# Kernel optimization log

Measured on AMD Instinct MI355X. Metric: run time of the kernel, lower is better.

Reference implementation:

```python
import jax, jax.numpy as jnp
import numpy as np
import math
from jax import lax

D_MODEL = 128
N_HEADS = 8
D_HEAD = D_MODEL // N_HEADS
D_FF = 4 * D_MODEL
KERNEL = 25  # moving_avg kernel size
N_LAYERS = 2
EPS = 1e-5


def moving_avg(x):
    # x: [B, L, D]; replicate-pad (KERNEL-1)//2 at both ends, window mean (AvgPool1d stride 1)
    p = (KERNEL - 1) // 2
    xp = jnp.concatenate([jnp.repeat(x[:, :1], p, axis=1), x, jnp.repeat(x[:, -1:], p, axis=1)], axis=1)
    s = lax.reduce_window(xp, 0.0, lax.add, (1, KERNEL, 1), (1, 1, 1), 'VALID')
    return s / KERNEL


def series_decomp(x):
    mm = moving_avg(x)
    return x - mm, mm


def autocorrelation(q, k, v):
    # q,k,v: [B, L, H, E]; FFT-based period correlation + top-k time-delay aggregation (training path)
    B, L, H, E = q.shape
    top_k = int(1 * math.log(L))  # factor=1
    qf = jnp.fft.rfft(q.transpose(0, 2, 3, 1), axis=-1)
    kf = jnp.fft.rfft(k.transpose(0, 2, 3, 1), axis=-1)
    corr = jnp.fft.irfft(qf * jnp.conj(kf), n=L, axis=-1)  # [B, H, E, L]
    vals = v.transpose(0, 2, 3, 1)                          # [B, H, E, L]
    mean_value = corr.mean(axis=(1, 2))                     # [B, L]
    _, index = lax.top_k(mean_value.mean(axis=0), top_k)    # [top_k], lags shared over batch
    weights = mean_value[:, index]                          # [B, top_k]
    tmp_corr = jax.nn.softmax(weights, axis=-1)
    agg = jnp.zeros_like(vals)
    for i in range(top_k):  # static small loop (top_k = 8)
        pattern = jnp.roll(vals, -index[i], axis=-1)
        agg = agg + pattern * tmp_corr[:, i][:, None, None, None]
    return agg.transpose(0, 3, 1, 2)  # [B, L, H, E]


def attn_layer(x, w, b):
    # w: [4, D, D] (q,k,v,out torch-Linear weights), b: [4, D]
    B, L, D = x.shape
    q = (jnp.einsum('bld,ed->ble', x, w[0]) + b[0]).reshape(B, L, N_HEADS, D_HEAD)
    k = (jnp.einsum('bld,ed->ble', x, w[1]) + b[1]).reshape(B, L, N_HEADS, D_HEAD)
    v = (jnp.einsum('bld,ed->ble', x, w[2]) + b[2]).reshape(B, L, N_HEADS, D_HEAD)
    o = autocorrelation(q, k, v).reshape(B, L, D)
    return jnp.einsum('bld,ed->ble', o, w[3]) + b[3]


def encoder_layer(x, w, b, w1, w2):
    x = x + attn_layer(x, w, b)
    x, _ = series_decomp(x)
    y = jax.nn.gelu(jnp.einsum('bld,fd->blf', x, w1), approximate=False)  # conv1 (k=1, no bias)
    y = jnp.einsum('blf,df->bld', y, w2)                                   # conv2 (k=1, no bias)
    res, _ = series_decomp(x + y)
    return res


def reference(x_enc, emb_w, attn_w, attn_b, ffn_w1, ffn_w2, norm_g, norm_b, fc1_w, fc1_b, fc2_w, fc2_b):
    # token embedding: Conv1d(C -> D, kernel 3, circular padding, no bias)
    xc = x_enc.transpose(0, 2, 1)  # [B, C, L]
    xc = jnp.concatenate([xc[:, :, -1:], xc, xc[:, :, :1]], axis=-1)
    h = lax.conv_general_dilated(xc, emb_w, (1,), 'VALID', dimension_numbers=('NCH', 'OIH', 'NCH'))
    h = h.transpose(0, 2, 1)  # [B, L, D]
    for l in range(N_LAYERS):
        h = encoder_layer(h, attn_w[l], attn_b[l], ffn_w1[l], ffn_w2[l])
    # my_Layernorm: LayerNorm then subtract time-mean
    mu = h.mean(axis=-1, keepdims=True)
    var = ((h - mu) ** 2).mean(axis=-1, keepdims=True)
    ln = (h - mu) / jnp.sqrt(var + EPS) * norm_g + norm_b
    h = ln - ln.mean(axis=1, keepdims=True)
    # head: gelu -> mean pool over time -> MLP
    h = jax.nn.gelu(h, approximate=False).mean(axis=1)  # [B, D]
    h = jax.nn.relu(jnp.einsum('bd,hd->bh', h, fc1_w) + fc1_b)
    return jnp.einsum('bh,ch->bc', h, fc2_w) + fc2_b


def setup_inputs() -> dict:
    key = jax.random.key(0)
    ks = jax.random.split(key, 8)
    B, L, C, NC, FC = 32, 4096, 12, 5, 128
    s = 0.02
    return {
        'x_enc': jax.random.normal(ks[0], (B, L, C), jnp.float32),
        'emb_w': jax.random.normal(ks[1], (D_MODEL, C, 3), jnp.float32) * s,
        'attn_w': jax.random.normal(ks[2], (N_LAYERS, 4, D_MODEL, D_MODEL), jnp.float32) * s,
        'attn_b': jnp.zeros((N_LAYERS, 4, D_MODEL), jnp.float32),
        'ffn_w1': jax.random.normal(ks[3], (N_LAYERS, D_FF, D_MODEL), jnp.float32) * s,
        'ffn_w2': jax.random.normal(ks[4], (N_LAYERS, D_MODEL, D_FF), jnp.float32) * s,
        'norm_g': jnp.ones((D_MODEL,), jnp.float32),
        'norm_b': jnp.zeros((D_MODEL,), jnp.float32),
        'fc1_w': jax.random.normal(ks[5], (FC, D_MODEL), jnp.float32) * s,
        'fc1_b': jnp.zeros((FC,), jnp.float32),
        'fc2_w': jax.random.normal(ks[6], (NC, FC), jnp.float32) * s,
        'fc2_b': jnp.zeros((NC,), jnp.float32),
    }
```

## Files before the change

### kernel.cpp

```cpp
#include <hip/hip_runtime.h>
#include <math.h>

#define L_SEQ 4096
#define BATCH 32
#define DM 128

typedef short short8 __attribute__((ext_vector_type(8)));
typedef short short4v __attribute__((ext_vector_type(4)));
typedef float f32x4 __attribute__((ext_vector_type(4)));

__device__ __forceinline__ float gelu_f(float x) {
    return 0.5f * x * (1.0f + erff(x * 0.70710678118654752f));
}
__device__ __forceinline__ float gelu_fast(float x) {
    float ax = fabsf(x);
    if (ax < 1.0f) {
        float z = x * 0.70710678118654752f;
        float z2 = z * z;
        float p = 1.0f + z2 * (-0.333333333f + z2 * (0.1f + z2 * (-0.0238095238f +
                  z2 * (4.62962963e-3f + z2 * (-7.57575758e-4f)))));
        return 0.5f * x * (1.0f + 1.1283791670955126f * z * p);
    }
    return 0.5f * x * (1.0f + erff(x * 0.70710678118654752f));
}
__device__ __forceinline__ unsigned short f2b(float f) {
    unsigned u = __float_as_uint(f);
    u += 0x7fffu + ((u >> 16) & 1u);
    return (unsigned short)(u >> 16);
}
__device__ __forceinline__ float b2f(unsigned short h) {
    return __uint_as_float(((unsigned)h) << 16);
}

__global__ __launch_bounds__(256) void kembed(const float* __restrict__ x,
                                              const float* __restrict__ w,
                                              float* __restrict__ h) {
    __shared__ float xs[130][12];
    __shared__ float wsm[128][37];
    int b = blockIdx.x >> 5;
    int lt = blockIdx.x & 31;
    int l0 = lt * 128;
    int tid = threadIdx.x;
    for (int i = tid; i < 130 * 12; i += 256) {
        int r = i / 12, c = i - r * 12;
        int gl = (l0 - 1 + r + 4096) & 4095;
        xs[r][c] = x[((size_t)b * 4096 + gl) * 12 + c];
    }
    for (int i = tid; i < 128 * 36; i += 256) {
        int o = i / 36, j = i - o * 36;
        wsm[o][j] = w[i];
    }
    __syncthreads();
    int o = tid & 127, lh = tid >> 7;
    float wr[36];
#pragma unroll
    for (int j = 0; j < 36; j++) wr[j] = wsm[o][j];
    int base_r = lh * 64;
    float ring[4][12];
#pragma unroll
    for (int c = 0; c < 12; c++) { ring[0][c] = xs[base_r][c]; ring[1][c] = xs[base_r + 1][c]; }
    float* hp = h + ((size_t)b * 4096 + l0 + lh * 64) * 128 + o;
#pragma unroll 4
    for (int st = 0; st < 64; st++) {
        int s0 = st & 3, s1 = (st + 1) & 3, s2 = (st + 2) & 3;
#pragma unroll
        for (int c = 0; c < 12; c++) ring[s2][c] = xs[base_r + st + 2][c];
        float s = 0.f;
#pragma unroll
        for (int c = 0; c < 12; c++)
            s += wr[c * 3 + 0] * ring[s0][c] + wr[c * 3 + 1] * ring[s1][c] + wr[c * 3 + 2] * ring[s2][c];
        hp[(size_t)st * 128] = s;
    }
}

__global__ __launch_bounds__(256) void kprepw(const float* __restrict__ w1,
                                              const float* __restrict__ w2,
                                              const float* __restrict__ attn_w,
                                              unsigned short* __restrict__ w1img,
                                              unsigned short* __restrict__ w2img,
                                              unsigned short* __restrict__ qkh,
                                              unsigned short* __restrict__ qkl,
                                              unsigned short* __restrict__ voimg) {
    int t = blockIdx.x * 256 + threadIdx.x;
    if (t < 262144) {
        int layer = t >> 17; int rem = t & 131071;
        if (rem < 65536) {
            int R = rem >> 7, x = rem & 127;
            int g = x >> 3, j = x & 7;
            int srcc = ((g ^ (R & 7)) << 3) + j;
            w1img[(size_t)layer * 65536 + rem] = f2b(w1[(size_t)layer * 65536 + R * 128 + srcc]);
        } else {
            int r2 = rem - 65536;
            int c = r2 >> 13; int D = (r2 >> 6) & 127; int x = r2 & 63;
            int g = x >> 3, j = x & 7;
            int srcf = c * 64 + ((g ^ (D & 7)) << 3) + j;
            w2img[(size_t)layer * 65536 + r2] = f2b(w2[(size_t)layer * 65536 + D * 512 + srcf]);
        }
    } else if (t < 327680) {
        int t2 = t - 262144;
        int layer = t2 >> 15; int rem = t2 & 32767;
        int y = rem >> 14; int rem2 = rem & 16383;
        int r64 = rem2 >> 7; int x = rem2 & 127;
        int r = r64 & 63;
        int g = x >> 3, j = x & 7;
        int srcc = ((g ^ (r & 7)) << 3) + j;
        float v = attn_w[(size_t)layer * 65536 + y * 16384 + r64 * 128 + srcc];
        unsigned short hh = f2b(v);
        qkh[t2] = hh;
        qkl[t2] = f2b(v - b2f(hh));
    } else {
        int t3 = t - 327680;
        int layer = t3 >> 15; int rem = t3 & 32767;
        int mat = rem >> 14; int rem2 = rem & 16383;
        int r = rem2 >> 7; int x = rem2 & 127;
        int g = x >> 3, j = x & 7;
        int srcc = ((g ^ (r & 7)) << 3) + j;
        voimg[t3] = f2b(attn_w[(size_t)layer * 65536 + (2 + mat) * 16384 + r * 128 + srcc]);
    }
}

__global__ __launch_bounds__(256, 2) void kgemm_qkb(const float* __restrict__ A,
                                                    const unsigned short* __restrict__ qkh,
                                                    const unsigned short* __restrict__ qkl,
                                                    const float* __restrict__ ab,
                                                    unsigned short* __restrict__ CTb) {
    __shared__ __align__(16) char smem[65536];
    short* Ah = (short*)smem;
    short* Al = (short*)(smem + 16384);
    short* Wh = (short*)(smem + 32768);
    short* Wl = (short*)(smem + 49152);
    int role = blockIdx.x;
    int y = role >> 1, half = role & 1;
    const unsigned short* wh = qkh + y * 16384 + half * 8192;
    const unsigned short* wl = qkl + y * 16384 + half * 8192;
    const float* bias = ab + y * 128 + half * 64;
    int row0 = blockIdx.y * 64;
    int tid = threadIdx.x;
#pragma unroll
    for (int u = 0; u < 4; u++) {
        int task = tid + u * 256;
        int r = task >> 4, cg = task & 15;
        int dst = r * 128 + ((cg ^ (r & 7)) << 3);
        const float* src = A + ((size_t)(row0 + r)) * 128 + cg * 8;
        float4 xa = *(const float4*)src, ya = *(const float4*)(src + 4);
        float av[8] = {xa.x, xa.y, xa.z, xa.w, ya.x, ya.y, ya.z, ya.w};
        short8 hi, lo;
#pragma unroll
        for (int j = 0; j < 8; j++) {
            unsigned short h = f2b(av[j]);
            hi[j] = (short)h; lo[j] = (short)f2b(av[j] - b2f(h));
        }
        *(short8*)(Ah + dst) = hi; *(short8*)(Al + dst) = lo;
        int lin = r * 128 + cg * 8;
        *(short8*)(Wh + lin) = *(const short8*)(wh + lin);
        *(short8*)(Wl + lin) = *(const short8*)(wl + lin);
    }
    __syncthreads();
    int l = tid & 63; int w = tid >> 6; int wm = w >> 1, wn = w & 1;
    f32x4 acc[2][2];
#pragma unroll
    for (int i = 0; i < 2; i++)
#pragma unroll
        for (int j = 0; j < 2; j++) acc[i][j] = (f32x4){0.f, 0.f, 0.f, 0.f};
#pragma unroll
    for (int ks = 0; ks < 4; ks++) {
        int cg = ks * 4 + (l >> 4);
        short8 ah[2], al2[2], bh[2], bl[2];
#pragma unroll
        for (int mi = 0; mi < 2; mi++) {
            int rm = wm * 32 + mi * 16 + (l & 15);
            int off = rm * 128 + ((cg ^ (rm & 7)) << 3);
            ah[mi] = *(short8*)(Ah + off); al2[mi] = *(short8*)(Al + off);
        }
#pragma unroll
        for (int ni = 0; ni < 2; ni++) {
            int rn = wn * 32 + ni * 16 + (l & 15);
            int off = rn * 128 + ((cg ^ (rn & 7)) << 3);
            bh[ni] = *(short8*)(Wh + off); bl[ni] = *(short8*)(Wl + off);
        }
#pragma unroll
        for (int mi = 0; mi < 2; mi++)
#pragma unroll
            for (int ni = 0; ni < 2; ni++) {
                acc[mi][ni] = __builtin_amdgcn_mfma_f32_16x16x32_bf16(ah[mi], bh[ni], acc[mi][ni], 0, 0, 0);
                acc[mi][ni] = __builtin_amdgcn_mfma_f32_16x16x32_bf16(ah[mi], bl[ni], acc[mi][ni], 0, 0, 0);
                acc[mi][ni] = __builtin_amdgcn_mfma_f32_16x16x32_bf16(al2[mi], bh[ni], acc[mi][ni], 0, 0, 0);
            }
    }
    __syncthreads();
    float* Dsh = (float*)smem;
#pragma unroll
    for (int mi = 0; mi < 2; mi++)
#pragma unroll
        for (int ni = 0; ni < 2; ni++)
#pragma unroll
            for (int rr = 0; rr < 4; rr++) {
                int m = wm * 32 + mi * 16 + (l >> 4) * 4 + rr;
                int n = wn * 32 + ni * 16 + (l & 15);
                Dsh[n * 68 + m] = acc[mi][ni][rr] + bias[n];
            }
    __syncthreads();
    int b = row0 >> 12; int l0 = row0 & 4095;
    int cb = y * 128 + half * 64;
#pragma unroll
    for (int u = 0; u < 4; u++) {
        int task = tid + u * 256;
        int c = task >> 4, m4 = (task & 15) * 4;
        float4 v = *(float4*)&Dsh[c * 68 + m4];
        short4v o;
        o[0] = (short)f2b(v.x); o[1] = (short)f2b(v.y);
        o[2] = (short)f2b(v.z); o[3] = (short)f2b(v.w);
        *(short4v*)&CTb[((size_t)(b * 256 + cb + c)) * 4096 + l0 + m4] = o;
    }
}

template <int AT, int EPI>
__global__ __launch_bounds__(256, 2) void kgemm_mfma(const void* __restrict__ Ap,
                                                     const unsigned short* __restrict__ Wimg,
                                                     const float* __restrict__ bias,
                                                     const float* __restrict__ res,
                                                     const float* __restrict__ tcb,
                                                     const int* __restrict__ idxb,
                                                     void* __restrict__ outp) {
    __shared__ __align__(16) char smem[65536];
    short* As = (short*)smem;
    short* Ws = (short*)(smem + 32768);
    int tid = threadIdx.x;
    size_t row0 = (size_t)blockIdx.x * 128;
#pragma unroll
    for (int u = 0; u < 8; u++) {
        int g = tid + u * 256;
        int r = g >> 4, cg = g & 15;
        int dsti = r * 128 + ((cg ^ (r & 7)) << 3);
        short8 v;
        if (AT == 0) {
            const float* src = (const float*)Ap + (row0 + r) * 128 + cg * 8;
            float4 x = *(const float4*)src, y = *(const float4*)(src + 4);
            v[0] = f2b(x.x); v[1] = f2b(x.y); v[2] = f2b(x.z); v[3] = f2b(x.w);
            v[4] = f2b(y.x); v[5] = f2b(y.y); v[6] = f2b(y.z); v[7] = f2b(y.w);
        } else {
            const unsigned short* Vb = (const unsigned short*)Ap;
            int b = (int)(row0 >> 12);
            int l0 = (int)(row0 & 4095);
            float accv[8];
#pragma unroll
            for (int j = 0; j < 8; j++) accv[j] = 0.f;
#pragma unroll
            for (int i = 0; i < 8; i++) {
                float wgt = tcb[b * 8 + i];
                int lr = (l0 + r + idxb[i]) & 4095;
                short8 vv = *(const short8*)(Vb + ((size_t)(b * 4096 + lr)) * 128 + cg * 8);
#pragma unroll
                for (int j = 0; j < 8; j++) accv[j] += wgt * b2f((unsigned short)vv[j]);
            }
#pragma unroll
            for (int j = 0; j < 8; j++) v[j] = (short)f2b(accv[j]);
        }
        *(short8*)(As + dsti) = v;
        int lin = r * 128 + cg * 8;
        *(short8*)(Ws + lin) = *(const short8*)(Wimg + lin);
    }
    __syncthreads();
    int l = tid & 63; int w = tid >> 6; int wm = w >> 1, wn = w & 1;
    f32x4 acc[4][4];
#pragma unroll
    for (int i = 0; i < 4; i++)
#pragma unroll
        for (int j = 0; j < 4; j++) acc[i][j] = (f32x4){0.f, 0.f, 0.f, 0.f};
#pragma unroll
    for (int ks = 0; ks < 4; ks++) {
        int cg = ks * 4 + (l >> 4);
        short8 af[4], bf[4];
#pragma unroll
        for (int mi = 0; mi < 4; mi++) {
            int rm = wm * 64 + mi * 16 + (l & 15);
            af[mi] = *(short8*)(As + rm * 128 + ((cg ^ (rm & 7)) << 3));
        }
#pragma unroll
        for (int ni = 0; ni < 4; ni++) {
            int rn = wn * 64 + ni * 16 + (l & 15);
            bf[ni] = *(short8*)(Ws + rn * 128 + ((cg ^ (rn & 7)) << 3));
        }
#pragma unroll
        for (int mi = 0; mi < 4; mi++)
#pragma unroll
            for (int ni = 0; ni < 4; ni++)
                acc[mi][ni] = __builtin_amdgcn_mfma_f32_16x16x32_bf16(af[mi], bf[ni], acc[mi][ni], 0, 0, 0);
    }
    __syncthreads();
    float* Dsh = (float*)smem;
#pragma unroll
    for (int mi = 0; mi < 4; mi++)
#pragma unroll
        for (int ni = 0; ni < 4; ni++)
#pragma unroll
            for (int rr = 0; rr < 4; rr++)
                Dsh[(wm * 64 + mi * 16 + (l >> 4) * 4 + rr) * 128 + wn * 64 + ni * 16 + (l & 15)] = acc[mi][ni][rr];
    __syncthreads();
#pragma unroll
    for (int u = 0; u < 8; u++) {
        int g = tid + u * 256;
        int r = g >> 4, c8 = (g & 15) * 8;
        float vv[8];
#pragma unroll
        for (int j = 0; j < 8; j++) vv[j] = Dsh[r * 128 + c8 + j] + bias[c8 + j];
        if (EPI == 1) {
            const float* rp = res + (row0 + r) * 128 + c8;
#pragma unroll
            for (int j = 0; j < 8; j++) vv[j] += rp[j];
            float* op = (float*)outp + (row0 + r) * 128 + c8;
            *(float4*)op = make_float4(vv[0], vv[1], vv[2], vv[3]);
            *(float4*)(op + 4) = make_float4(vv[4], vv[5], vv[6], vv[7]);
        } else {
            short8 ov;
#pragma unroll
            for (int j = 0; j < 8; j++) ov[j] = (short)f2b(vv[j]);
            *(short8*)((short*)outp + (row0 + r) * 128 + c8) = ov;
        }
    }
}

#define LOADW(FB) do { \
    _Pragma("unroll") \
    for (int u = 0; u < 4; u++) { \
        int task = tid + u * 256; \
        int r = task >> 4, cg = task & 15; \
        p1[u] = *(const short8*)(w1img + ((size_t)((FB) * 64 + r)) * 128 + cg * 8); \
        int r2 = task >> 3, cg2 = task & 7; \
        p2[u] = *(const short8*)(w2img + ((size_t)((FB) * 128 + r2)) * 64 + cg2 * 8); \
    } \
} while (0)

__global__ __launch_bounds__(256, 2) void kffn_mfma(const float* __restrict__ xs,
                                                    const unsigned short* __restrict__ w1img,
                                                    const unsigned short* __restrict__ w2img,
                                                    float* __restrict__ outp) {
    __shared__ __align__(16) char smem[81920];
    short* xsl = (short*)smem;
    short* w1t = (short*)(smem + 32768);
    short* tt  = (short*)(smem + 49152);
    short* w2t = (short*)(smem + 65536);
    int tid = threadIdx.x;
    size_t row0 = (size_t)blockIdx.x * 128;
#pragma unroll
    for (int u = 0; u < 8; u++) {
        int g = tid + u * 256;
        int r = g >> 4, cg = g & 15;
        const float* src = xs + (row0 + r) * 128 + cg * 8;
        float4 x = *(const float4*)src, y = *(const float4*)(src + 4);
        short8 v;
        v[0] = f2b(x.x); v[1] = f2b(x.y); v[2] = f2b(x.z); v[3] = f2b(x.w);
        v[4] = f2b(y.x); v[5] = f2b(y.y); v[6] = f2b(y.z); v[7] = f2b(y.w);
        *(short8*)(xsl + r * 128 + ((cg ^ (r & 7)) << 3)) = v;
    }
    int l = tid & 63; int w = tid >> 6; int wm = w >> 1, wn = w & 1;
    f32x4 acc2[4][4];
#pragma unroll
    for (int i = 0; i < 4; i++)
#pragma unroll
        for (int j = 0; j < 4; j++) acc2[i][j] = (f32x4){0.f, 0.f, 0.f, 0.f};
    short8 p1[4], p2[4];
    LOADW(0);
    for (int fb = 0; fb < 8; fb++) {
        __syncthreads();
#pragma unroll
        for (int u = 0; u < 4; u++) {
            int task = tid + u * 256;
            int r = task >> 4, cg = task & 15;
            *(short8*)(w1t + r * 128 + cg * 8) = p1[u];
            int r2 = task >> 3, cg2 = task & 7;
            *(short8*)(w2t + r2 * 64 + cg2 * 8) = p2[u];
        }
        __syncthreads();
        if (fb < 7) LOADW(fb + 1);
        f32x4 a1[4][2];
#pragma unroll
        for (int i = 0; i < 4; i++)
#pragma unroll
            for (int j = 0; j < 2; j++) a1[i][j] = (f32x4){0.f, 0.f, 0.f, 0.f};
#pragma unroll
        for (int ks = 0; ks < 4; ks++) {
            int cg = ks * 4 + (l >> 4);
            short8 af[4], bf[2];
#pragma unroll
            for (int mi = 0; mi < 4; mi++) {
                int rm = wm * 64 + mi * 16 + (l & 15);
                af[mi] = *(short8*)(xsl + rm * 128 + ((cg ^ (rm & 7)) << 3));
            }
#pragma unroll
            for (int ni = 0; ni < 2; ni++) {
                int rn = wn * 32 + ni * 16 + (l & 15);
                bf[ni] = *(short8*)(w1t + rn * 128 + ((cg ^ (rn & 7)) << 3));
            }
#pragma unroll
            for (int mi = 0; mi < 4; mi++)
#pragma unroll
                for (int ni = 0; ni < 2; ni++)
                    a1[mi][ni] = __builtin_amdgcn_mfma_f32_16x16x32_bf16(af[mi], bf[ni], a1[mi][ni], 0, 0, 0);
        }
#pragma unroll
        for (int mi = 0; mi < 4; mi++)
#pragma unroll
            for (int ni = 0; ni < 2; ni++)
#pragma unroll
                for (int rr = 0; rr < 4; rr++) {
                    int m = wm * 64 + mi * 16 + (l >> 4) * 4 + rr;
                    int f = wn * 32 + ni * 16 + (l & 15);
                    tt[m * 64 + (((f >> 3) ^ (m & 7)) << 3) + (f & 7)] = (short)f2b(gelu_fast(a1[mi][ni][rr]));
                }
        __syncthreads();
#pragma unroll
        for (int ks = 0; ks < 2; ks++) {
            int cg = ks * 4 + (l >> 4);
            short8 af[4], bf[4];
#pragma unroll
            for (int mi = 0; mi < 4; mi++) {
                int rm = wm * 64 + mi * 16 + (l & 15);
                af[mi] = *(short8*)(tt + rm * 64 + ((cg ^ (rm & 7)) << 3));
            }
#pragma unroll
            for (int ni = 0; ni < 4; ni++) {
                int rn = wn * 64 + ni * 16 + (l & 15);
                bf[ni] = *(short8*)(w2t + rn * 64 + ((cg ^ (rn & 7)) << 3));
            }
#pragma unroll
            for (int mi = 0; mi < 4; mi++)
#pragma unroll
                for (int ni = 0; ni < 4; ni++)
                    acc2[mi][ni] = __builtin_amdgcn_mfma_f32_16x16x32_bf16(af[mi], bf[ni], acc2[mi][ni], 0, 0, 0);
        }
    }
    __syncthreads();
    float* Dsh = (float*)smem;
#pragma unroll
    for (int mi = 0; mi < 4; mi++)
#pragma unroll
        for (int ni = 0; ni < 4; ni++)
#pragma unroll
            for (int rr = 0; rr < 4; rr++)
                Dsh[(wm * 64 + mi * 16 + (l >> 4) * 4 + rr) * 128 + wn * 64 + ni * 16 + (l & 15)] = acc2[mi][ni][rr];
    __syncthreads();
#pragma unroll
    for (int u = 0; u < 8; u++) {
        int g = tid + u * 256;
        int r = g >> 4, c8 = (g & 15) * 8;
        const float* rp = xs + (row0 + r) * 128 + c8;
        float* op = outp + (row0 + r) * 128 + c8;
        float4 o0, o1;
        o0.x = Dsh[r * 128 + c8 + 0] + rp[0]; o0.y = Dsh[r * 128 + c8 + 1] + rp[1];
        o0.z = Dsh[r * 128 + c8 + 2] + rp[2]; o0.w = Dsh[r * 128 + c8 + 3] + rp[3];
        o1.x = Dsh[r * 128 + c8 + 4] + rp[4]; o1.y = Dsh[r * 128 + c8 + 5] + rp[5];
        o1.z = Dsh[r * 128 + c8 + 6] + rp[6]; o1.w = Dsh[r * 128 + c8 + 7] + rp[7];
        *(float4*)op = o0; *(float4*)(op + 4) = o1;
    }
}

#define FIDX(a) ((a) + ((a) >> 4))

__device__ __forceinline__ float2 twget(const float2* __restrict__ tw, int a, float sgn) {
    float2 T = tw[a & 1023];
    int hi = (a >> 10) & 3;
    float cs = (hi & 1) ? ((hi & 2) ? T.y : -T.y) : ((hi & 2) ? -T.x : T.x);
    float sn = (hi & 1) ? ((hi & 2) ? -T.x : T.x) : ((hi & 2) ? -T.y : T.y);
    return make_float2(cs, sn * sgn);
}

__device__ void fft4096_r4(float2* __restrict__ b0, float2* __restrict__ b1,
                           const float2* __restrict__ tw, float sgn, int tid) {
    float2* cur = b0; float2* nxt = b1;
#pragma unroll
    for (int t = 0; t < 6; t++) {
        int s = 1 << (t << 1);
        int q = tid & (s - 1);
        int ps = tid - q;
        float2 a0 = cur[FIDX(tid)];
        float2 a1 = cur[FIDX(tid + 1024)];
        float2 a2 = cur[FIDX(tid + 2048)];
        float2 a3 = cur[FIDX(tid + 3072)];
        float t0x = a0.x + a2.x, t0y = a0.y + a2.y;
        float t1x = a0.x - a2.x, t1y = a0.y - a2.y;
        float t2x = a1.x + a3.x, t2y = a1.y + a3.y;
        float t3x = a1.x - a3.x, t3y = a1.y - a3.y;
        float it3x = -sgn * t3y, it3y = sgn * t3x;
        float2 A0 = make_float2(t0x + t2x, t0y + t2y);
        float2 A1 = make_float2(t1x + it3x, t1y + it3y);
        float2 A2 = make_float2(t0x - t2x, t0y - t2y);
        float2 A3 = make_float2(t1x - it3x, t1y - it3y);
        int ob = q + (ps << 2);
        nxt[FIDX(ob)] = A0;
        float2 w1 = twget(tw, ps, sgn);
        float2 w2 = twget(tw, ps * 2, sgn);
        float2 w3 = twget(tw, ps * 3, sgn);
        nxt[FIDX(ob + s)] = make_float2(A1.x * w1.x - A1.y * w1.y, A1.x * w1.y + A1.y * w1.x);
        nxt[FIDX(ob + 2 * s)] = make_float2(A2.x * w2.x - A2.y * w2.y, A2.x * w2.y + A2.y * w2.x);
        nxt[FIDX(ob + 3 * s)] = make_float2(A3.x * w3.x - A3.y * w3.y, A3.x * w3.y + A3.y * w3.x);
        __syncthreads();
        float2* tp = cur; cur = nxt; nxt = tp;
    }
}

__global__ __launch_bounds__(1024) void kfft_fwd(const unsigned short* __restrict__ qkT,
                                                 float* __restrict__ Pws) {
    __shared__ float2 bufA[4352];
    __shared__ float2 bufB[4352];
    __shared__ float2 tw[1024];
    int tid = threadIdx.x;
    {
        float sn, cs;
        sincosf(1.5339807878856412e-3f * (float)tid, &sn, &cs);
        tw[tid] = make_float2(cs, sn);
    }
    int b = blockIdx.x >> 4;
    int g = blockIdx.x & 15;
    float2 pacc[4];
#pragma unroll
    for (int j = 0; j < 4; j++) pacc[j] = make_float2(0.f, 0.f);
    for (int c8 = 0; c8 < 8; c8++) {
        int c = g * 8 + c8;
        const unsigned short* qrow = qkT + ((size_t)(b * 256 + c)) * 4096;
        const unsigned short* krow = qkT + ((size_t)(b * 256 + 128 + c)) * 4096;
        __syncthreads();
        int i0 = tid * 4;
        short4v qv = *(const short4v*)(qrow + i0);
        short4v kv = *(const short4v*)(krow + i0);
        bufA[FIDX(i0)]     = make_float2(b2f((unsigned short)qv[0]), b2f((unsigned short)kv[0]));
        bufA[FIDX(i0 + 1)] = make_float2(b2f((unsigned short)qv[1]), b2f((unsigned short)kv[1]));
        bufA[FIDX(i0 + 2)] = make_float2(b2f((unsigned short)qv[2]), b2f((unsigned short)kv[2]));
        bufA[FIDX(i0 + 3)] = make_float2(b2f((unsigned short)qv[3]), b2f((unsigned short)kv[3]));
        __syncthreads();
        fft4096_r4(bufA, bufB, tw, -1.f, tid);
#pragma unroll
        for (int j = 0; j < 4; j++) {
            int f = tid + j * 1024;
            float2 Zf = bufA[FIDX(f)];
            float2 Zm = bufA[FIDX((4096 - f) & 4095)];
            float Qre = 0.5f * (Zf.x + Zm.x), Qim = 0.5f * (Zf.y - Zm.y);
            float Kre = 0.5f * (Zf.y + Zm.y), Kim = -0.5f * (Zf.x - Zm.x);
            pacc[j].x += Qre * Kre + Qim * Kim;
            pacc[j].y += Qim * Kre - Qre * Kim;
        }
    }
    float2* P = (float2*)Pws + (size_t)(b * 16 + g) * 4096;
#pragma unroll
    for (int j = 0; j < 4; j++) { int f = tid + j * 1024; P[f] = pacc[j]; }
}

__global__ __launch_bounds__(1024) void kfft_inv(const float* __restrict__ Pws,
                                                 float* __restrict__ meanv) {
    __shared__ float2 bufA[4352];
    __shared__ float2 bufB[4352];
    __shared__ float2 tw[1024];
    int tid = threadIdx.x;
    {
        float sn, cs;
        sincosf(1.5339807878856412e-3f * (float)tid, &sn, &cs);
        tw[tid] = make_float2(cs, sn);
    }
    int b = blockIdx.x;
    const float2* P = (const float2*)Pws + (size_t)b * 16 * 4096;
#pragma unroll
    for (int j = 0; j < 4; j++) {
        int i = tid + j * 1024;
        float2 s = make_float2(0.f, 0.f);
#pragma unroll
        for (int gg = 0; gg < 16; gg++) { float2 v = P[gg * 4096 + i]; s.x += v.x; s.y += v.y; }
        bufA[FIDX(i)] = s;
    }
    __syncthreads();
    fft4096_r4(bufA, bufB, tw, 1.f, tid);
    const float scale = 1.0f / (4096.0f * 128.0f);
#pragma unroll
    for (int j = 0; j < 4; j++) {
        int i = tid + j * 1024;
        meanv[b * 4096 + i] = bufA[FIDX(i)].x * scale;
    }
}

__global__ __launch_bounds__(256) void kcolsum(const float* __restrict__ meanv,
                                               float* __restrict__ cmg) {
    int c = blockIdx.x * 256 + threadIdx.x;
    float s = 0.f;
    for (int b = 0; b < 32; b++) s += meanv[b * 4096 + c];
    cmg[c] = s;
}

__global__ __launch_bounds__(256) void ktopk2(const float* __restrict__ cmg,
                                              const float* __restrict__ meanv,
                                              int* __restrict__ idxout,
                                              float* __restrict__ tc) {
    __shared__ float cm[4096];
    __shared__ float rv[256];
    __shared__ int ri[256];
    __shared__ int sidx[8];
    for (int c = threadIdx.x; c < 4096; c += 256) cm[c] = cmg[c];
    __syncthreads();
    for (int it = 0; it < 8; it++) {
        float bv = -1e30f; int bi = 0;
        for (int c = threadIdx.x; c < 4096; c += 256) {
            float v = cm[c];
            if (v > bv) { bv = v; bi = c; }
        }
        rv[threadIdx.x] = bv; ri[threadIdx.x] = bi;
        __syncthreads();
        for (int off = 128; off > 0; off >>= 1) {
            if (threadIdx.x < off) {
                float v2 = rv[threadIdx.x + off]; int i2 = ri[threadIdx.x + off];
                if (v2 > rv[threadIdx.x] || (v2 == rv[threadIdx.x] && i2 < ri[threadIdx.x])) {
                    rv[threadIdx.x] = v2; ri[threadIdx.x] = i2;
                }
            }
            __syncthreads();
        }
        if (threadIdx.x == 0) { sidx[it] = ri[0]; idxout[it] = ri[0]; cm[ri[0]] = -1e30f; }
        __syncthreads();
    }
    if (threadIdx.x < 32) {
        int b = threadIdx.x;
        float w[8]; float mx = -1e30f;
#pragma unroll
        for (int i = 0; i < 8; i++) { w[i] = meanv[b * 4096 + sidx[i]]; mx = fmaxf(mx, w[i]); }
        float s = 0.f;
#pragma unroll
        for (int i = 0; i < 8; i++) { w[i] = expf(w[i] - mx); s += w[i]; }
#pragma unroll
        for (int i = 0; i < 8; i++) tc[b * 8 + i] = w[i] / s;
    }
}

__global__ __launch_bounds__(256) void kdecomp(const float* __restrict__ in,
                                               float* __restrict__ outp) {
    int b = blockIdx.x >> 4; int lc = blockIdx.x & 15;
    int dg = threadIdx.x & 31; int ls = threadIdx.x >> 5;
    int l0 = lc * 256 + ls * 32;
    const float* base = in + (size_t)b * 524288 + dg * 4;
    float* ob = outp + (size_t)b * 524288 + dg * 4;
    float sx = 0.f, sy = 0.f, sz = 0.f, sw = 0.f;
#pragma unroll
    for (int j = -12; j <= 12; j++) {
        int lj = l0 + j;
        lj = lj < 0 ? 0 : (lj > 4095 ? 4095 : lj);
        float4 v = *(const float4*)(base + (size_t)lj * 128);
        sx += v.x; sy += v.y; sz += v.z; sw += v.w;
    }
    for (int st = 0; st < 32; st++) {
        int l = l0 + st;
        float4 c = *(const float4*)(base + (size_t)l * 128);
        float4 o = make_float4(c.x - sx * (1.0f / 25.0f), c.y - sy * (1.0f / 25.0f),
                               c.z - sz * (1.0f / 25.0f), c.w - sw * (1.0f / 25.0f));
        *(float4*)(ob + (size_t)l * 128) = o;
        int ln = l + 13 > 4095 ? 4095 : l + 13;
        int lo2 = l - 12 < 0 ? 0 : l - 12;
        float4 vn = *(const float4*)(base + (size_t)ln * 128);
        float4 vo = *(const float4*)(base + (size_t)lo2 * 128);
        sx += vn.x - vo.x; sy += vn.y - vo.y; sz += vn.z - vo.z; sw += vn.w - vo.w;
    }
}

__global__ __launch_bounds__(256) void kln_part1(float* __restrict__ h,
                                                 const float* __restrict__ g,
                                                 const float* __restrict__ bb,
                                                 float* __restrict__ part) {
    __shared__ float sh[4][128];
    int b = blockIdx.x >> 5;
    int sl = blockIdx.x & 31;
    int w = threadIdx.x >> 6;
    int lane = threadIdx.x & 63;
    float2 gv = *(const float2*)(g + lane * 2);
    float2 bv = *(const float2*)(bb + lane * 2);
    size_t r0 = (size_t)b * 4096 + sl * 128 + w * 32;
    float c0 = 0.f, c1 = 0.f;
    for (int i = 0; i < 32; i++) {
        float* p = h + (r0 + i) * 128 + lane * 2;
        float2 v = *(float2*)p;
        float s = v.x + v.y, s2 = v.x * v.x + v.y * v.y;
#pragma unroll
        for (int off = 32; off; off >>= 1) { s += __shfl_down(s, off); s2 += __shfl_down(s2, off); }
        s = __shfl(s, 0); s2 = __shfl(s2, 0);
        float mu = s * (1.f / 128.f);
        float var = s2 * (1.f / 128.f) - mu * mu;
        float inv = rsqrtf(var + 1e-5f);
        float o0 = (v.x - mu) * inv * gv.x + bv.x;
        float o1 = (v.y - mu) * inv * gv.y + bv.y;
        *(float2*)p = make_float2(o0, o1);
        c0 += o0; c1 += o1;
    }
    sh[w][lane * 2] = c0; sh[w][lane * 2 + 1] = c1;
    __syncthreads();
    if (threadIdx.x < 128) {
        int d = threadIdx.x;
        part[(size_t)(b * 32 + sl) * 128 + d] = sh[0][d] + sh[1][d] + sh[2][d] + sh[3][d];
    }
}

__global__ __launch_bounds__(128) void kpart2(const float* __restrict__ part,
                                              float* __restrict__ outm, int nq) {
    int b = blockIdx.x; int d = threadIdx.x;
    float s = 0.f;
    for (int q = 0; q < nq; q++) s += part[(size_t)(b * nq + q) * 128 + d];
    outm[b * 128 + d] = s * (1.f / 4096.f);
}

__global__ __launch_bounds__(256) void kgpart1(const float* __restrict__ h,
                                               const float* __restrict__ msum,
                                               float* __restrict__ part) {
    int b = blockIdx.x >> 3, sl = blockIdx.x & 7;
    int d = threadIdx.x & 127, p = threadIdx.x >> 7;
    const float* base = h + ((size_t)b * 4096 + sl * 512) * 128;
    float m = msum[b * 128 + d];
    float acc = 0.f;
    for (int l = p; l < 512; l += 2) acc += gelu_f(base[(size_t)l * 128 + d] - m);
    __shared__ float sh[256];
    sh[threadIdx.x] = acc; __syncthreads();
    if (p == 0) part[(size_t)(b * 8 + sl) * 128 + d] = acc + sh[128 + d];
}

__global__ __launch_bounds__(256) void khead(const float* __restrict__ gmean,
                                             const float* __restrict__ fc1w,
                                             const float* __restrict__ fc1b,
                                             const float* __restrict__ fc2w,
                                             const float* __restrict__ fc2b,
                                             float* __restrict__ outp) {
    __shared__ float h0[32][128];
    __shared__ float h1[32][128];
    int tid = threadIdx.x;
#pragma unroll
    for (int i = 0; i < 16; i++) {
        int e = tid + i * 256;
        h0[e >> 7][e & 127] = gmean[e];
    }
    __syncthreads();
#pragma unroll
    for (int i = 0; i < 16; i++) {
        int e = tid + i * 256; int b = e >> 7, j = e & 127;
        float s = fc1b[j];
        for (int d = 0; d < 128; d++) s += h0[b][d] * fc1w[j * 128 + d];
        h1[b][j] = fmaxf(s, 0.f);
    }
    __syncthreads();
    if (tid < 160) {
        int b = tid / 5, c2 = tid % 5;
        float s = fc2b[c2];
        for (int j = 0; j < 128; j++) s += h1[b][j] * fc2w[c2 * 128 + j];
        outp[b * 5 + c2] = s;
    }
}

extern "C" void kernel_launch(void* const* d_in, const int* in_sizes, int n_in,
                              void* d_out, int out_size, void* d_ws, size_t ws_size,
                              hipStream_t stream) {
    const float* x_enc  = (const float*)d_in[0];
    const float* emb_w  = (const float*)d_in[1];
    const float* attn_w = (const float*)d_in[2];
    const float* attn_b = (const float*)d_in[3];
    const float* ffn_w1 = (const float*)d_in[4];
    const float* ffn_w2 = (const float*)d_in[5];
    const float* norm_g = (const float*)d_in[6];
    const float* norm_b = (const float*)d_in[7];
    const float* fc1_w  = (const float*)d_in[8];
    const float* fc1_b  = (const float*)d_in[9];
    const float* fc2_w  = (const float*)d_in[10];
    const float* fc2_b  = (const float*)d_in[11];
    float* outp = (float*)d_out;

    float* W = (float*)d_ws;
    const size_t RD = (size_t)BATCH * L_SEQ * DM;
    float* buf0  = W;
    float* buf1  = W + RD;
    float* Pws   = W + 2 * RD;
    float* meanv = Pws + (size_t)4194304;
    float* tcb   = meanv + (size_t)131072;
    int*   idxb  = (int*)(tcb + 256);
    float* part  = tcb + 256 + 64;
    float* msum  = part + 32768;
    float* gsum  = msum + 4096;
    unsigned short* w1img = (unsigned short*)(gsum + 4096);
    unsigned short* w2img = w1img + (size_t)2 * 65536;
    unsigned short* qkh   = w2img + (size_t)2 * 65536;
    unsigned short* qkl   = qkh + (size_t)65536;
    unsigned short* voimg = qkl + (size_t)65536;
    float* cmg   = (float*)(voimg + (size_t)65536);

    kembed<<<1024, 256, 0, stream>>>(x_enc, emb_w, buf0);
    kprepw<<<1536, 256, 0, stream>>>(ffn_w1, ffn_w2, attn_w, w1img, w2img, qkh, qkl, voimg);

    float* H = buf0;
    float* S = buf1;
    for (int l = 0; l < 2; l++) {
        const float* ab = attn_b + (size_t)l * 4 * 128;
        unsigned short* CTb = (unsigned short*)S;
        kgemm_qkb<<<dim3(4, 2048), 256, 0, stream>>>(H, qkh + (size_t)l * 32768,
                                                     qkl + (size_t)l * 32768, ab, CTb);
        kfft_fwd<<<512, 1024, 0, stream>>>(CTb, Pws);
        kfft_inv<<<32, 1024, 0, stream>>>(Pws, meanv);
        kcolsum<<<16, 256, 0, stream>>>(meanv, cmg);
        ktopk2<<<1, 256, 0, stream>>>(cmg, meanv, idxb, tcb);
        unsigned short* Vb = (unsigned short*)S;
        kgemm_mfma<0, 0><<<1024, 256, 0, stream>>>(H, voimg + (size_t)l * 32768, ab + 256,
                                                   nullptr, nullptr, nullptr, Vb);
        kgemm_mfma<2, 1><<<1024, 256, 0, stream>>>(Vb, voimg + (size_t)l * 32768 + 16384, ab + 384,
                                                   H, tcb, idxb, H);
        kdecomp<<<512, 256, 0, stream>>>(H, S);
        kffn_mfma<<<1024, 256, 0, stream>>>(S, w1img + (size_t)l * 65536,
                                            w2img + (size_t)l * 65536, H);
        kdecomp<<<512, 256, 0, stream>>>(H, S);
        float* t = H; H = S; S = t;
    }

    kln_part1<<<1024, 256, 0, stream>>>(H, norm_g, norm_b, meanv);
    kpart2<<<32, 128, 0, stream>>>(meanv, msum, 32);
    kgpart1<<<256, 256, 0, stream>>>(H, msum, part);
    kpart2<<<32, 128, 0, stream>>>(part, gsum, 8);
    khead<<<1, 256, 0, stream>>>(gsum, fc1_w, fc1_b, fc2_w, fc2_b, outp);
}
```

Measured before the change: 1.010 ms.

## Reuse A tile across QK roles, split psum reduction, remap AV blocks, drop FFN prefetch

```diff
diff --git a/kernel.cpp b/kernel.cpp
--- a/kernel.cpp
+++ b/kernel.cpp
@@ -129,88 +129,94 @@
     short* Al = (short*)(smem + 16384);
     short* Wh = (short*)(smem + 32768);
     short* Wl = (short*)(smem + 49152);
-    int role = blockIdx.x;
-    int y = role >> 1, half = role & 1;
-    const unsigned short* wh = qkh + y * 16384 + half * 8192;
-    const unsigned short* wl = qkl + y * 16384 + half * 8192;
-    const float* bias = ab + y * 128 + half * 64;
-    int row0 = blockIdx.y * 64;
+    float* Dsh = (float*)(smem + 32768);
+    int row0i = blockIdx.x * 64;
     int tid = threadIdx.x;
 #pragma unroll
     for (int u = 0; u < 4; u++) {
         int task = tid + u * 256;
         int r = task >> 4, cg = task & 15;
         int dst = r * 128 + ((cg ^ (r & 7)) << 3);
-        const float* src = A + ((size_t)(row0 + r)) * 128 + cg * 8;
+        const float* src = A + ((size_t)(row0i + r)) * 128 + cg * 8;
         float4 xa = *(const float4*)src, ya = *(const float4*)(src + 4);
         float av[8] = {xa.x, xa.y, xa.z, xa.w, ya.x, ya.y, ya.z, ya.w};
         short8 hi, lo;
 #pragma unroll
         for (int j = 0; j < 8; j++) {
-            unsigned short h = f2b(av[j]);
-            hi[j] = (short)h; lo[j] = (short)f2b(av[j] - b2f(h));
+            unsigned short hh = f2b(av[j]);
+            hi[j] = (short)hh; lo[j] = (short)f2b(av[j] - b2f(hh));
         }
         *(short8*)(Ah + dst) = hi; *(short8*)(Al + dst) = lo;
-        int lin = r * 128 + cg * 8;
-        *(short8*)(Wh + lin) = *(const short8*)(wh + lin);
-        *(short8*)(Wl + lin) = *(const short8*)(wl + lin);
-    }
-    __syncthreads();
+    }
     int l = tid & 63; int w = tid >> 6; int wm = w >> 1, wn = w & 1;
-    f32x4 acc[2][2];
-#pragma unroll
-    for (int i = 0; i < 2; i++)
-#pragma unroll
-        for (int j = 0; j < 2; j++) acc[i][j] = (f32x4){0.f, 0.f, 0.f, 0.f};
-#pragma unroll
-    for (int ks = 0; ks < 4; ks++) {
-        int cg = ks * 4 + (l >> 4);
-        short8 ah[2], al2[2], bh[2], bl[2];
-#pragma unroll
-        for (int mi = 0; mi < 2; mi++) {
-            int rm = wm * 32 + mi * 16 + (l & 15);
-            int off = rm * 128 + ((cg ^ (rm & 7)) << 3);
-            ah[mi] = *(short8*)(Ah + off); al2[mi] = *(short8*)(Al + off);
-        }
-#pragma unroll
-        for (int ni = 0; ni < 2; ni++) {
-            int rn = wn * 32 + ni * 16 + (l & 15);
-            int off = rn * 128 + ((cg ^ (rn & 7)) << 3);
-            bh[ni] = *(short8*)(Wh + off); bl[ni] = *(short8*)(Wl + off);
-        }
+    int b = row0i >> 12; int l0 = row0i & 4095;
+    for (int role = 0; role < 4; role++) {
+        int y = role >> 1, half = role & 1;
+        const unsigned short* wh = qkh + y * 16384 + half * 8192;
+        const unsigned short* wl = qkl + y * 16384 + half * 8192;
+        const float* bias = ab + y * 128 + half * 64;
+        __syncthreads();
+#pragma unroll
+        for (int u = 0; u < 4; u++) {
+            int task = tid + u * 256;
+            int lin = (task >> 4) * 128 + (task & 15) * 8;
+            *(short8*)(Wh + lin) = *(const short8*)(wh + lin);
+            *(short8*)(Wl + lin) = *(const short8*)(wl + lin);
+        }
+        __syncthreads();
+        f32x4 acc[2][2];
+#pragma unroll
+        for (int i = 0; i < 2; i++)
+#pragma unroll
+            for (int j = 0; j < 2; j++) acc[i][j] = (f32x4){0.f, 0.f, 0.f, 0.f};
+#pragma unroll
+        for (int ks = 0; ks < 4; ks++) {
+            int cg = ks * 4 + (l >> 4);
+            short8 ah[2], al2[2], bh[2], bl[2];
+#pragma unroll
+            for (int mi = 0; mi < 2; mi++) {
+                int rm = wm * 32 + mi * 16 + (l & 15);
+                int off = rm * 128 + ((cg ^ (rm & 7)) << 3);
+                ah[mi] = *(short8*)(Ah + off); al2[mi] = *(short8*)(Al + off);
+            }
+#pragma unroll
+            for (int ni = 0; ni < 2; ni++) {
+                int rn = wn * 32 + ni * 16 + (l & 15);
+                int off = rn * 128 + ((cg ^ (rn & 7)) << 3);
+                bh[ni] = *(short8*)(Wh + off); bl[ni] = *(short8*)(Wl + off);
+            }
+#pragma unroll
+            for (int mi = 0; mi < 2; mi++)
+#pragma unroll
+                for (int ni = 0; ni < 2; ni++) {
+                    acc[mi][ni] = __builtin_amdgcn_mfma_f32_16x16x32_bf16(ah[mi], bh[ni], acc[mi][ni], 0, 0, 0);
+                    acc[mi][ni] = __builtin_amdgcn_mfma_f32_16x16x32_bf16(ah[mi], bl[ni], acc[mi][ni], 0, 0, 0);
+                    acc[mi][ni] = __builtin_amdgcn_mfma_f32_16x16x32_bf16(al2[mi], bh[ni], acc[mi][ni], 0, 0, 0);
+                }
+        }
+        __syncthreads();
 #pragma unroll
         for (int mi = 0; mi < 2; mi++)
 #pragma unroll
-            for (int ni = 0; ni < 2; ni++) {
-                acc[mi][ni] = __builtin_amdgcn_mfma_f32_16x16x32_bf16(ah[mi], bh[ni], acc[mi][ni], 0, 0, 0);
-                acc[mi][ni] = __builtin_amdgcn_mfma_f32_16x16x32_bf16(ah[mi], bl[ni], acc[mi][ni], 0, 0, 0);
-                acc[mi][ni] = __builtin_amdgcn_mfma_f32_16x16x32_bf16(al2[mi], bh[ni], acc[mi][ni], 0, 0, 0);
-            }
-    }
-    __syncthreads();
-    float* Dsh = (float*)smem;
-#pragma unroll
-    for (int mi = 0; mi < 2; mi++)
-#pragma unroll
-        for (int ni = 0; ni < 2; ni++)
-#pragma unroll
-            for (int rr = 0; rr < 4; rr++) {
-                int m = wm * 32 + mi * 16 + (l >> 4) * 4 + rr;
-                int n = wn * 32 + ni * 16 + (l & 15);
-                Dsh[n * 68 + m] = acc[mi][ni][rr] + bias[n];
-            }
-    __syncthreads();
-    int b = row0 >> 12; int l0 = row0 & 4095;
-    int cb = y * 128 + half * 64;
-#pragma unroll
-    for (int u = 0; u < 4; u++) {
-        int task = tid + u * 256;
-        int c = task >> 4, m4 = (task & 15) * 4;
-        float4 v = *(float4*)&Dsh[c * 68 + m4];
-        short4v o;
-        o[0] = (short)f2b(v.x); o[1] = (short)f2b(v.y);
-        o[2] = (short)f2b(v.z); o[3] = (short)f2b(v.w);
-        *(short4v*)&CTb[((size_t)(b * 256 + cb + c)) * 4096 + l0 + m4] = o;
+            for (int ni = 0; ni < 2; ni++)
+#pragma unroll
+                for (int rr = 0; rr < 4; rr++) {
+                    int m = wm * 32 + mi * 16 + (l >> 4) * 4 + rr;
+                    int n = wn * 32 + ni * 16 + (l & 15);
+                    Dsh[n * 68 + m] = acc[mi][ni][rr] + bias[n];
+                }
+        __syncthreads();
+        int cb = y * 128 + half * 64;
+#pragma unroll
+        for (int u = 0; u < 4; u++) {
+            int task = tid + u * 256;
+            int c = task >> 4, m4 = (task & 15) * 4;
+            float4 v = *(float4*)&Dsh[c * 68 + m4];
+            short4v o;
+            o[0] = (short)f2b(v.x); o[1] = (short)f2b(v.y);
+            o[2] = (short)f2b(v.z); o[3] = (short)f2b(v.w);
+            *(short4v*)&CTb[((size_t)(b * 256 + cb + c)) * 4096 + l0 + m4] = o;
+        }
     }
 }
 
@@ -226,7 +232,16 @@
     short* As = (short*)smem;
     short* Ws = (short*)(smem + 32768);
     int tid = threadIdx.x;
-    size_t row0 = (size_t)blockIdx.x * 128;
+    size_t row0;
+    if (AT == 2) {
+        int B = blockIdx.x;
+        int cls = B & 7, j = B >> 3;
+        int bq = cls + 8 * (j >> 5);
+        int t = j & 31;
+        row0 = ((size_t)bq * 32 + t) * 128;
+    } else {
+        row0 = (size_t)blockIdx.x * 128;
+    }
 #pragma unroll
     for (int u = 0; u < 8; u++) {
         int g = tid + u * 256;
@@ -320,17 +335,6 @@
     }
 }
 
-#define LOADW(FB) do { \
-    _Pragma("unroll") \
-    for (int u = 0; u < 4; u++) { \
-        int task = tid + u * 256; \
-        int r = task >> 4, cg = task & 15; \
-        p1[u] = *(const short8*)(w1img + ((size_t)((FB) * 64 + r)) * 128 + cg * 8); \
-        int r2 = task >> 3, cg2 = task & 7; \
-        p2[u] = *(const short8*)(w2img + ((size_t)((FB) * 128 + r2)) * 64 + cg2 * 8); \
-    } \
-} while (0)
-
 __global__ __launch_bounds__(256, 2) void kffn_mfma(const float* __restrict__ xs,
                                                     const unsigned short* __restrict__ w1img,
                                                     const unsigned short* __restrict__ w2img,
@@ -359,20 +363,19 @@
     for (int i = 0; i < 4; i++)
 #pragma unroll
         for (int j = 0; j < 4; j++) acc2[i][j] = (f32x4){0.f, 0.f, 0.f, 0.f};
-    short8 p1[4], p2[4];
-    LOADW(0);
     for (int fb = 0; fb < 8; fb++) {
         __syncthreads();
 #pragma unroll
         for (int u = 0; u < 4; u++) {
             int task = tid + u * 256;
             int r = task >> 4, cg = task & 15;
-            *(short8*)(w1t + r * 128 + cg * 8) = p1[u];
+            *(short8*)(w1t + r * 128 + cg * 8) =
+                *(const short8*)(w1img + ((size_t)(fb * 64 + r)) * 128 + cg * 8);
             int r2 = task >> 3, cg2 = task & 7;
-            *(short8*)(w2t + r2 * 64 + cg2 * 8) = p2[u];
-        }
-        __syncthreads();
-        if (fb < 7) LOADW(fb + 1);
+            *(short8*)(w2t + r2 * 64 + cg2 * 8) =
+                *(const short8*)(w2img + ((size_t)(fb * 128 + r2)) * 64 + cg2 * 8);
+        }
+        __syncthreads();
         f32x4 a1[4][2];
 #pragma unroll
         for (int i = 0; i < 4; i++)
@@ -545,7 +548,21 @@
     for (int j = 0; j < 4; j++) { int f = tid + j * 1024; P[f] = pacc[j]; }
 }
 
-__global__ __launch_bounds__(1024) void kfft_inv(const float* __restrict__ Pws,
+__global__ __launch_bounds__(256) void kpsum(const float* __restrict__ Pws,
+                                             float* __restrict__ Pr) {
+    int t = blockIdx.x * 256 + threadIdx.x;
+    int b = t >> 12, i = t & 4095;
+    const float2* P = (const float2*)Pws;
+    float2 s = make_float2(0.f, 0.f);
+#pragma unroll
+    for (int gg = 0; gg < 16; gg++) {
+        float2 v = P[((size_t)(b * 16 + gg)) * 4096 + i];
+        s.x += v.x; s.y += v.y;
+    }
+    ((float2*)Pr)[(size_t)b * 4096 + i] = s;
+}
+
+__global__ __launch_bounds__(1024) void kfft_inv(const float* __restrict__ Prs,
                                                  float* __restrict__ meanv) {
     __shared__ float2 bufA[4352];
     __shared__ float2 bufB[4352];
@@ -557,14 +574,11 @@
         tw[tid] = make_float2(cs, sn);
     }
     int b = blockIdx.x;
-    const float2* P = (const float2*)Pws + (size_t)b * 16 * 4096;
+    const float2* P = (const float2*)Prs + (size_t)b * 4096;
 #pragma unroll
     for (int j = 0; j < 4; j++) {
         int i = tid + j * 1024;
-        float2 s = make_float2(0.f, 0.f);
-#pragma unroll
-        for (int gg = 0; gg < 16; gg++) { float2 v = P[gg * 4096 + i]; s.x += v.x; s.y += v.y; }
-        bufA[FIDX(i)] = s;
+        bufA[FIDX(i)] = P[i];
     }
     __syncthreads();
     fft4096_r4(bufA, bufB, tw, 1.f, tid);
@@ -779,6 +793,7 @@
     unsigned short* qkl   = qkh + (size_t)65536;
     unsigned short* voimg = qkl + (size_t)65536;
     float* cmg   = (float*)(voimg + (size_t)65536);
+    float* Pr    = cmg + 4096;
 
     kembed<<<1024, 256, 0, stream>>>(x_enc, emb_w, buf0);
     kprepw<<<1536, 256, 0, stream>>>(ffn_w1, ffn_w2, attn_w, w1img, w2img, qkh, qkl, voimg);
@@ -788,10 +803,11 @@
     for (int l = 0; l < 2; l++) {
         const float* ab = attn_b + (size_t)l * 4 * 128;
         unsigned short* CTb = (unsigned short*)S;
-        kgemm_qkb<<<dim3(4, 2048), 256, 0, stream>>>(H, qkh + (size_t)l * 32768,
-                                                     qkl + (size_t)l * 32768, ab, CTb);
+        kgemm_qkb<<<2048, 256, 0, stream>>>(H, qkh + (size_t)l * 32768,
+                                            qkl + (size_t)l * 32768, ab, CTb);
         kfft_fwd<<<512, 1024, 0, stream>>>(CTb, Pws);
-        kfft_inv<<<32, 1024, 0, stream>>>(Pws, meanv);
+        kpsum<<<512, 256, 0, stream>>>(Pws, Pr);
+        kfft_inv<<<32, 1024, 0, stream>>>(Pr, meanv);
         kcolsum<<<16, 256, 0, stream>>>(meanv, cmg);
         ktopk2<<<1, 256, 0, stream>>>(cmg, meanv, idxb, tcb);
         unsigned short* Vb = (unsigned short*)S;
```

After: 990.1 us. No clear change (-1.9%).
